# Optimization experiments

Measured on AMD Instinct MI355X. Metric: run time of the kernel, lower is better.

The kernel has to match this reference:

```python
import jax, jax.numpy as jnp
import numpy as np

EPS = 1e-8

def setup_inputs() -> dict:
    key = jax.random.key(0)
    ks = jax.random.split(key, 7)
    B, S, H, NH, V = 4, 2048, 1024, 8, 2048
    sc = 1.0 / np.sqrt(H)
    return {
        "hidden": jax.random.normal(ks[0], (B, S, H), jnp.float32),
        "prior_w": jax.random.normal(ks[1], (H, NH), jnp.float32) * sc,
        "prior_b": jnp.zeros((NH,), jnp.float32),
        "latent_w": jax.random.normal(ks[2], (H, NH * H), jnp.float32) * sc,
        "latent_b": jnp.zeros((NH * H,), jnp.float32),
        "output_w": jax.random.normal(ks[3], (H, V), jnp.float32) * sc,
        "output_b": jnp.zeros((V,), jnp.float32),
    }

def reference(hidden, prior_w, prior_b, latent_w, latent_b, output_w, output_b):
    B, S, H = hidden.shape
    NH = prior_w.shape[1]
    # prior: sigmoid then renormalize over heads
    prior = jax.nn.sigmoid(hidden @ prior_w + prior_b)              # [B,S,NH]
    prior = prior / (prior.sum(-1, keepdims=True) + EPS)
    # latent: linear -> [B,S,NH,H] -> tanh
    latent = jnp.tanh((hidden @ latent_w + latent_b).reshape(B, S, NH, H))
    # per-head softmax over vocab, weighted sum over heads
    logits = jnp.einsum('bsnh,hv->bsnv', latent, output_w) + output_b
    probs = jax.nn.softmax(logits, axis=-1)                          # [B,S,NH,V]
    return jnp.einsum('bsn,bsnv->bsv', prior, probs)
```

## Files before the change

kernel.cpp:

```cpp
#include <hip/hip_runtime.h>
#include <hip/hip_bf16.h>
#include <stdint.h>

typedef _Float16 f16;
typedef _Float16 f16x8 __attribute__((ext_vector_type(8)));
typedef _Float16 f16x4 __attribute__((ext_vector_type(4)));
typedef float f32x4 __attribute__((ext_vector_type(4)));

#define T_TOK 8192
#define H_DIM 1024
#define NHEAD 8
#define V_DIM 2048

__device__ __forceinline__ void gload16(const void* g, void* l) {
  __builtin_amdgcn_global_load_lds(
      (const __attribute__((address_space(1))) void*)(uintptr_t)g,
      (__attribute__((address_space(3))) void*)(unsigned)(uintptr_t)l,
      16, 0, 0);
}

__device__ __forceinline__ float fast_tanh(float x) {
  float xc = fminf(fmaxf(x, -12.f), 12.f);
  float e = __expf(2.f * xc);
  return (e - 1.f) / (e + 1.f);
}

__device__ __forceinline__ void stage_half(const f16* __restrict__ gRowBase,
                                           char* ldsHalf, int tid, int sl8,
                                           int Kd) {
  const int srow = tid >> 3;
  char* wuni = ldsHalf + ((tid >> 6) << 10);
  gload16(gRowBase + (size_t)srow * Kd + sl8, wuni);
  gload16(gRowBase + (size_t)(srow + 64) * Kd + sl8, wuni + 8192);
}

template <int TANH>
__global__ __launch_bounds__(512, 2) void k_gemm(const f16* __restrict__ A,
                                                 const f16* __restrict__ Bt,
                                                 const float* __restrict__ bias,
                                                 f16* __restrict__ C,
                                                 int M, int N, int K) {
  __shared__ __align__(16) f16 sA[2][16384];
  __shared__ __align__(16) f16 sB[2][16384];
  const int tid = threadIdx.x;
  const int lane = tid & 63;
  const int wid = tid >> 6;
  const int wr = wid >> 2, wc = wid & 3;
  const int m0 = blockIdx.y * 256, n0 = blockIdx.x * 256;
  const int NT = K >> 6;
  const int sl8 = ((tid & 7) ^ ((tid >> 3) & 7)) << 3;
  const int lo15 = lane & 15;
  const int offk0 = lo15 * 128 + (((lane >> 4)) ^ (lane & 7)) * 16;
  const int offk1 = lo15 * 128 + ((4 + (lane >> 4)) ^ (lane & 7)) * 16;

  const f16* Ag = A + (size_t)m0 * K;
  const f16* Bg = Bt + (size_t)n0 * K;
  char* sAb = (char*)&sA[0][0];
  char* sBb = (char*)&sB[0][0];

  stage_half(Ag, sAb, tid, sl8, K);
  stage_half(Ag + (size_t)128 * K, sAb + 16384, tid, sl8, K);
  stage_half(Bg, sBb, tid, sl8, K);
  stage_half(Bg + (size_t)128 * K, sBb + 16384, tid, sl8, K);
  stage_half(Bg + 64, sBb + 32768, tid, sl8, K);
  stage_half(Bg + (size_t)128 * K + 64, sBb + 32768 + 16384, tid, sl8, K);
  asm volatile("s_waitcnt vmcnt(4)" ::: "memory");
  __builtin_amdgcn_s_barrier();
  __builtin_amdgcn_sched_barrier(0);

  f32x4 acc[8][4] = {};
  f16x8 bf[4][2];

#define PHASE(q, STAGE_STMT)                                                   \
  {                                                                            \
    f16x8 af[2];                                                               \
    f16x8 af1[2];                                                              \
    if (q == 0) {                                                              \
      _Pragma("unroll") for (int ni = 0; ni < 4; ++ni) {                       \
        bf[ni][0] = *(const f16x8*)(cB + wc * 8192 + ni * 2048 + offk0);       \
        bf[ni][1] = *(const f16x8*)(cB + wc * 8192 + ni * 2048 + offk1);       \
      }                                                                        \
    }                                                                          \
    af[0] = *(const f16x8*)(cA + wr * 16384 + (2 * q + 0) * 2048 + offk0);     \
    af[1] = *(const f16x8*)(cA + wr * 16384 + (2 * q + 0) * 2048 + offk1);     \
    af1[0] = *(const f16x8*)(cA + wr * 16384 + (2 * q + 1) * 2048 + offk0);    \
    af1[1] = *(const f16x8*)(cA + wr * 16384 + (2 * q + 1) * 2048 + offk1);    \
    STAGE_STMT;                                                                \
    __builtin_amdgcn_s_barrier();                                              \
    asm volatile("s_waitcnt lgkmcnt(0)" ::: "memory");                         \
    __builtin_amdgcn_sched_barrier(0);                                         \
    __builtin_amdgcn_s_setprio(1);                                             \
    _Pragma("unroll") for (int ni = 0; ni < 4; ++ni) {                         \
      acc[2 * q + 0][ni] = __builtin_amdgcn_mfma_f32_16x16x32_f16(             \
          af[0], bf[ni][0], acc[2 * q + 0][ni], 0, 0, 0);                      \
      acc[2 * q + 0][ni] = __builtin_amdgcn_mfma_f32_16x16x32_f16(             \
          af[1], bf[ni][1], acc[2 * q + 0][ni], 0, 0, 0);                      \
      acc[2 * q + 1][ni] = __builtin_amdgcn_mfma_f32_16x16x32_f16(             \
          af1[0], bf[ni][0], acc[2 * q + 1][ni], 0, 0, 0);                     \
      acc[2 * q + 1][ni] = __builtin_amdgcn_mfma_f32_16x16x32_f16(             \
          af1[1], bf[ni][1], acc[2 * q + 1][ni], 0, 0, 0);                     \
    }                                                                          \
    __builtin_amdgcn_s_setprio(0);                                             \
  }

#pragma unroll 2
  for (int T = 0; T < NT; ++T) {
    const int buf = T & 1;
    const char* cA = sAb + buf * 32768;
    const char* cB = sBb + buf * 32768;
    char* nA = sAb + (buf ^ 1) * 32768;
    char* nB = sBb + buf * 32768;
    const int ktA = (T + 1) << 6;
    const int ktB = (T + 2) << 6;

    PHASE(0, { if (T + 1 < NT) stage_half(Ag + ktA, nA, tid, sl8, K); })
    __builtin_amdgcn_s_barrier();
    PHASE(1, { if (T + 1 < NT) stage_half(Ag + (size_t)128 * K + ktA, nA + 16384, tid, sl8, K); })
    __builtin_amdgcn_s_barrier();
    PHASE(2, { if (T + 2 < NT) stage_half(Bg + ktB, nB, tid, sl8, K); })
    __builtin_amdgcn_s_barrier();
    PHASE(3, { if (T + 2 < NT) stage_half(Bg + (size_t)128 * K + ktB, nB + 16384, tid, sl8, K); })
    if (T + 2 < NT) {
      asm volatile("s_waitcnt vmcnt(4)" ::: "memory");
    } else {
      asm volatile("s_waitcnt vmcnt(0)" ::: "memory");
    }
    __builtin_amdgcn_s_barrier();
    __builtin_amdgcn_sched_barrier(0);
  }
#undef PHASE

  const int crow = m0 + wr * 128 + ((lane >> 4) << 2);
  const int ccol0 = n0 + wc * 64 + lo15;
#pragma unroll
  for (int ni = 0; ni < 4; ++ni) {
    const int col = ccol0 + ni * 16;
    const float bv = bias[col];
#pragma unroll
    for (int mi = 0; mi < 8; ++mi) {
#pragma unroll
      for (int r = 0; r < 4; ++r) {
        float v = acc[mi][ni][r] + bv;
        if (TANH) v = fast_tanh(v);
        C[(size_t)(crow + mi * 16 + r) * N + col] = (f16)v;
      }
    }
  }
}

__global__ __launch_bounds__(256) void k_convert(const float* __restrict__ in,
                                                 f16* __restrict__ out, int n4) {
  int i = blockIdx.x * blockDim.x + threadIdx.x;
  if (i >= n4) return;
  const float4 v = ((const float4*)in)[i];
  f16x4 o;
  o[0] = (f16)v.x; o[1] = (f16)v.y; o[2] = (f16)v.z; o[3] = (f16)v.w;
  ((f16x4*)out)[i] = o;
}

__global__ void k_transpose(const float* __restrict__ in, f16* __restrict__ out,
                            int R, int C) {
  __shared__ f16 tile[32][33];
  int c0 = blockIdx.x * 32, r0 = blockIdx.y * 32;
  for (int j = threadIdx.y; j < 32; j += 8)
    tile[j][threadIdx.x] = (f16)in[(size_t)(r0 + j) * C + (c0 + threadIdx.x)];
  __syncthreads();
  for (int j = threadIdx.y; j < 32; j += 8)
    out[(size_t)(c0 + j) * R + (r0 + threadIdx.x)] = tile[threadIdx.x][j];
}

__global__ __launch_bounds__(256) void k_prior(const float* __restrict__ hidden,
                                               const float* __restrict__ pw,
                                               const float* __restrict__ pb,
                                               float* __restrict__ prior) {
  const int wid = threadIdx.x >> 6, lane = threadIdx.x & 63;
  const int t = blockIdx.x * 4 + wid;
  float acc[NHEAD] = {0.f, 0.f, 0.f, 0.f, 0.f, 0.f, 0.f, 0.f};
  const float* hrow = hidden + (size_t)t * H_DIM;
  for (int k = lane; k < H_DIM; k += 64) {
    float x = hrow[k];
    const float* wr = pw + k * NHEAD;
#pragma unroll
    for (int h = 0; h < NHEAD; ++h) acc[h] += x * wr[h];
  }
#pragma unroll
  for (int h = 0; h < NHEAD; ++h) {
#pragma unroll
    for (int off = 32; off >= 1; off >>= 1) acc[h] += __shfl_xor(acc[h], off);
  }
  if (lane == 0) {
    float p[NHEAD], s = 0.f;
#pragma unroll
    for (int h = 0; h < NHEAD; ++h) {
      p[h] = 1.f / (1.f + __expf(-(acc[h] + pb[h])));
      s += p[h];
    }
    float inv = 1.f / (s + 1e-8f);
#pragma unroll
    for (int h = 0; h < NHEAD; ++h) prior[t * NHEAD + h] = p[h] * inv;
  }
}

__global__ __launch_bounds__(256) void k_softmax(const f16* __restrict__ logits,
                                                 const float* __restrict__ prior,
                                                 float* __restrict__ out) {
  __shared__ float red[4];
  const int t = blockIdx.x;
  const int tid = threadIdx.x, lane = tid & 63, wid = tid >> 6;
  float oa[8] = {0.f, 0.f, 0.f, 0.f, 0.f, 0.f, 0.f, 0.f};
  const int v0 = tid * 8;
#pragma unroll 1
  for (int h = 0; h < NHEAD; ++h) {
    f16x8 x = *(const f16x8*)(logits + ((size_t)t * NHEAD + h) * V_DIM + v0);
    float xv[8], mx = -1e30f;
#pragma unroll
    for (int j = 0; j < 8; j++) { xv[j] = (float)x[j]; mx = fmaxf(mx, xv[j]); }
#pragma unroll
    for (int off = 32; off >= 1; off >>= 1) mx = fmaxf(mx, __shfl_xor(mx, off));
    if (lane == 0) red[wid] = mx;
    __syncthreads();
    mx = fmaxf(fmaxf(red[0], red[1]), fmaxf(red[2], red[3]));
    __syncthreads();
    float e[8], s = 0.f;
#pragma unroll
    for (int j = 0; j < 8; j++) { e[j] = __expf(xv[j] - mx); s += e[j]; }
#pragma unroll
    for (int off = 32; off >= 1; off >>= 1) s += __shfl_xor(s, off);
    if (lane == 0) red[wid] = s;
    __syncthreads();
    s = red[0] + red[1] + red[2] + red[3];
    __syncthreads();
    const float coef = prior[t * NHEAD + h] / s;
#pragma unroll
    for (int j = 0; j < 8; j++) oa[j] += coef * e[j];
  }
  float4* op = (float4*)(out + (size_t)t * V_DIM + v0);
  op[0] = make_float4(oa[0], oa[1], oa[2], oa[3]);
  op[1] = make_float4(oa[4], oa[5], oa[6], oa[7]);
}

extern "C" void kernel_launch(void* const* d_in, const int* in_sizes, int n_in,
                              void* d_out, int out_size, void* d_ws, size_t ws_size,
                              hipStream_t stream) {
  const float* hidden   = (const float*)d_in[0];
  const float* prior_w  = (const float*)d_in[1];
  const float* prior_b  = (const float*)d_in[2];
  const float* latent_w = (const float*)d_in[3];
  const float* latent_b = (const float*)d_in[4];
  const float* output_w = (const float*)d_in[5];
  const float* output_b = (const float*)d_in[6];
  float* out = (float*)d_out;

  char* ws = (char*)d_ws;
  size_t off = 0;
  auto alloc = [&](size_t bytes) -> void* {
    void* p = ws + off;
    off += (bytes + 255) & ~(size_t)255;
    return p;
  };
  f16* hidden_h = (f16*)alloc((size_t)T_TOK * H_DIM * 2);
  f16* lw_t     = (f16*)alloc((size_t)NHEAD * H_DIM * H_DIM * 2);
  f16* ow_t     = (f16*)alloc((size_t)V_DIM * H_DIM * 2);
  float* prior  = (float*)alloc((size_t)T_TOK * NHEAD * 4);

  int tc = 2048;
  while (tc > 256) {
    size_t need = off + (size_t)tc * NHEAD * H_DIM * 2 + 256 +
                  (size_t)tc * NHEAD * V_DIM * 2 + 256;
    if (need <= ws_size) break;
    tc >>= 1;
  }
  f16* latent_h = (f16*)alloc((size_t)tc * NHEAD * H_DIM * 2);
  f16* logits_h = (f16*)alloc((size_t)tc * NHEAD * V_DIM * 2);

  k_convert<<<(T_TOK * H_DIM / 4 + 255) / 256, 256, 0, stream>>>(
      hidden, hidden_h, T_TOK * H_DIM / 4);
  k_transpose<<<dim3(NHEAD * H_DIM / 32, H_DIM / 32), dim3(32, 8), 0, stream>>>(
      latent_w, lw_t, H_DIM, NHEAD * H_DIM);
  k_transpose<<<dim3(V_DIM / 32, H_DIM / 32), dim3(32, 8), 0, stream>>>(
      output_w, ow_t, H_DIM, V_DIM);
  k_prior<<<T_TOK / 4, 256, 0, stream>>>(hidden, prior_w, prior_b, prior);

  const int nchunk = T_TOK / tc;
  for (int c = 0; c < nchunk; ++c) {
    const f16* Ah = hidden_h + (size_t)c * tc * H_DIM;
    k_gemm<1><<<dim3(NHEAD * H_DIM / 256, tc / 256), 512, 0, stream>>>(
        Ah, lw_t, latent_b, latent_h, tc, NHEAD * H_DIM, H_DIM);
    k_gemm<0><<<dim3(V_DIM / 256, tc * NHEAD / 256), 512, 0, stream>>>(
        latent_h, ow_t, output_b, logits_h, tc * NHEAD, V_DIM, H_DIM);
    k_softmax<<<tc, 256, 0, stream>>>(logits_h, prior + (size_t)c * tc * NHEAD,
                                      out + (size_t)c * tc * V_DIM);
  }
}
```

Before: 625.5 us.

## Software-pipeline LDS fragment loads across MFMA phases and swizzle block order

Restructures the GEMM main loop so the A fragments for the next phase are read from LDS while the current phase's MFMAs run, using double register sets (af0/af1), with the next tile's first A set prefetched after the tile barrier. This removes the per-phase lgkmcnt(0) wait that previously stalled the MFMAs. It also remaps block IDs with a stride-8 swizzle, intended to improve L2 locality across XCDs, and reorders the epilogue stores row-major. The cost is higher register pressure from the extra fragment set, and the loop assumes an even number of K tiles.

```diff
diff --git a/kernel.cpp b/kernel.cpp
--- a/kernel.cpp
+++ b/kernel.cpp
@@ -46,7 +46,11 @@
   const int lane = tid & 63;
   const int wid = tid >> 6;
   const int wr = wid >> 2, wc = wid & 3;
-  const int m0 = blockIdx.y * 256, n0 = blockIdx.x * 256;
+  const int gx = gridDim.x;
+  const int id = blockIdx.y * gx + blockIdx.x;
+  const int cpx = (gx * gridDim.y) >> 3;
+  const int sw = (id & 7) * cpx + (id >> 3);
+  const int m0 = (sw / gx) * 256, n0 = (sw % gx) * 256;
   const int NT = K >> 6;
   const int sl8 = ((tid & 7) ^ ((tid >> 3) & 7)) << 3;
   const int lo15 = lane & 15;
@@ -69,80 +73,106 @@
   __builtin_amdgcn_sched_barrier(0);
 
   f32x4 acc[8][4] = {};
-  f16x8 bf[4][2];
-
-#define PHASE(q, STAGE_STMT)                                                   \
+  f16x8 af0[4], af1[4], bf[4][2];
+
+#define LDA_SET(dst, base, q)                                                  \
   {                                                                            \
-    f16x8 af[2];                                                               \
-    f16x8 af1[2];                                                              \
-    if (q == 0) {                                                              \
-      _Pragma("unroll") for (int ni = 0; ni < 4; ++ni) {                       \
-        bf[ni][0] = *(const f16x8*)(cB + wc * 8192 + ni * 2048 + offk0);       \
-        bf[ni][1] = *(const f16x8*)(cB + wc * 8192 + ni * 2048 + offk1);       \
-      }                                                                        \
+    dst[0] = *(const f16x8*)((base) + wr * 16384 + (2 * (q) + 0) * 2048 + offk0); \
+    dst[1] = *(const f16x8*)((base) + wr * 16384 + (2 * (q) + 0) * 2048 + offk1); \
+    dst[2] = *(const f16x8*)((base) + wr * 16384 + (2 * (q) + 1) * 2048 + offk0); \
+    dst[3] = *(const f16x8*)((base) + wr * 16384 + (2 * (q) + 1) * 2048 + offk1); \
+  }
+#define LDB(base)                                                              \
+  {                                                                            \
+    _Pragma("unroll") for (int ni = 0; ni < 4; ++ni) {                         \
+      bf[ni][0] = *(const f16x8*)((base) + wc * 8192 + ni * 2048 + offk0);     \
+      bf[ni][1] = *(const f16x8*)((base) + wc * 8192 + ni * 2048 + offk1);     \
     }                                                                          \
-    af[0] = *(const f16x8*)(cA + wr * 16384 + (2 * q + 0) * 2048 + offk0);     \
-    af[1] = *(const f16x8*)(cA + wr * 16384 + (2 * q + 0) * 2048 + offk1);     \
-    af1[0] = *(const f16x8*)(cA + wr * 16384 + (2 * q + 1) * 2048 + offk0);    \
-    af1[1] = *(const f16x8*)(cA + wr * 16384 + (2 * q + 1) * 2048 + offk1);    \
-    STAGE_STMT;                                                                \
-    __builtin_amdgcn_s_barrier();                                              \
-    asm volatile("s_waitcnt lgkmcnt(0)" ::: "memory");                         \
-    __builtin_amdgcn_sched_barrier(0);                                         \
+  }
+#define MFMA16(q, S)                                                           \
+  {                                                                            \
     __builtin_amdgcn_s_setprio(1);                                             \
     _Pragma("unroll") for (int ni = 0; ni < 4; ++ni) {                         \
-      acc[2 * q + 0][ni] = __builtin_amdgcn_mfma_f32_16x16x32_f16(             \
-          af[0], bf[ni][0], acc[2 * q + 0][ni], 0, 0, 0);                      \
-      acc[2 * q + 0][ni] = __builtin_amdgcn_mfma_f32_16x16x32_f16(             \
-          af[1], bf[ni][1], acc[2 * q + 0][ni], 0, 0, 0);                      \
-      acc[2 * q + 1][ni] = __builtin_amdgcn_mfma_f32_16x16x32_f16(             \
-          af1[0], bf[ni][0], acc[2 * q + 1][ni], 0, 0, 0);                     \
-      acc[2 * q + 1][ni] = __builtin_amdgcn_mfma_f32_16x16x32_f16(             \
-          af1[1], bf[ni][1], acc[2 * q + 1][ni], 0, 0, 0);                     \
+      acc[2 * (q) + 0][ni] = __builtin_amdgcn_mfma_f32_16x16x32_f16(           \
+          S[0], bf[ni][0], acc[2 * (q) + 0][ni], 0, 0, 0);                     \
+      acc[2 * (q) + 0][ni] = __builtin_amdgcn_mfma_f32_16x16x32_f16(           \
+          S[1], bf[ni][1], acc[2 * (q) + 0][ni], 0, 0, 0);                     \
+      acc[2 * (q) + 1][ni] = __builtin_amdgcn_mfma_f32_16x16x32_f16(           \
+          S[2], bf[ni][0], acc[2 * (q) + 1][ni], 0, 0, 0);                     \
+      acc[2 * (q) + 1][ni] = __builtin_amdgcn_mfma_f32_16x16x32_f16(           \
+          S[3], bf[ni][1], acc[2 * (q) + 1][ni], 0, 0, 0);                     \
     }                                                                          \
     __builtin_amdgcn_s_setprio(0);                                             \
   }
 
-#pragma unroll 2
-  for (int T = 0; T < NT; ++T) {
-    const int buf = T & 1;
-    const char* cA = sAb + buf * 32768;
-    const char* cB = sBb + buf * 32768;
-    char* nA = sAb + (buf ^ 1) * 32768;
-    char* nB = sBb + buf * 32768;
-    const int ktA = (T + 1) << 6;
-    const int ktB = (T + 2) << 6;
-
-    PHASE(0, { if (T + 1 < NT) stage_half(Ag + ktA, nA, tid, sl8, K); })
-    __builtin_amdgcn_s_barrier();
-    PHASE(1, { if (T + 1 < NT) stage_half(Ag + (size_t)128 * K + ktA, nA + 16384, tid, sl8, K); })
-    __builtin_amdgcn_s_barrier();
-    PHASE(2, { if (T + 2 < NT) stage_half(Bg + ktB, nB, tid, sl8, K); })
-    __builtin_amdgcn_s_barrier();
-    PHASE(3, { if (T + 2 < NT) stage_half(Bg + (size_t)128 * K + ktB, nB + 16384, tid, sl8, K); })
-    if (T + 2 < NT) {
-      asm volatile("s_waitcnt vmcnt(4)" ::: "memory");
-    } else {
-      asm volatile("s_waitcnt vmcnt(0)" ::: "memory");
-    }
-    __builtin_amdgcn_s_barrier();
-    __builtin_amdgcn_sched_barrier(0);
-  }
-#undef PHASE
+  LDA_SET(af0, sAb, 0);
+
+#define HALF(tt, bc)                                                           \
+  {                                                                            \
+    const char* cA = sAb + (bc)*32768;                                         \
+    const char* cB = sBb + (bc)*32768;                                         \
+    char* nA = sAb + ((bc) ^ 1) * 32768;                                       \
+    char* nB = sBb + (bc)*32768;                                               \
+    const int ktA = ((tt) + 1) << 6, ktB = ((tt) + 2) << 6;                    \
+    const bool doA = (tt) + 1 < NT, doB = (tt) + 2 < NT;                       \
+                                    \
+    if (doA) stage_half(Ag + ktA, nA, tid, sl8, K);                            \
+    LDB(cB);                                                                   \
+    LDA_SET(af1, cA, 1);                                                       \
+    __builtin_amdgcn_sched_barrier(0);                                         \
+    MFMA16(0, af0);                                                            \
+    __builtin_amdgcn_s_barrier();                                              \
+                                                                      \
+    if (doA) stage_half(Ag + (size_t)128 * K + ktA, nA + 16384, tid, sl8, K);  \
+    LDA_SET(af0, cA, 2);                                                       \
+    __builtin_amdgcn_sched_barrier(0);                                         \
+    MFMA16(1, af1);                                                            \
+    __builtin_amdgcn_s_barrier();                                              \
+                                                                      \
+    if (doB) stage_half(Bg + ktB, nB, tid, sl8, K);                            \
+    LDA_SET(af1, cA, 3);                                                       \
+    __builtin_amdgcn_sched_barrier(0);                                         \
+    MFMA16(2, af0);                                                            \
+    __builtin_amdgcn_s_barrier();                                              \
+                  \
+    if (doB) stage_half(Bg + (size_t)128 * K + ktB, nB + 16384, tid, sl8, K);  \
+    if (doB) {                                                                 \
+      asm volatile("s_waitcnt vmcnt(4)" ::: "memory");                         \
+    } else {                                                                   \
+      asm volatile("s_waitcnt vmcnt(0)" ::: "memory");                         \
+    }                                                                          \
+    __builtin_amdgcn_s_barrier();                                              \
+    __builtin_amdgcn_sched_barrier(0);                                         \
+    if (doA) LDA_SET(af0, sAb + ((bc) ^ 1) * 32768, 0);                        \
+    __builtin_amdgcn_sched_barrier(0);                                         \
+    MFMA16(3, af1);                                                            \
+  }
+
+#pragma unroll 1
+  for (int T = 0; T < NT; T += 2) {
+    HALF(T, 0);
+    HALF(T + 1, 1);
+  }
+#undef HALF
+#undef LDA_SET
+#undef LDB
+#undef MFMA16
 
   const int crow = m0 + wr * 128 + ((lane >> 4) << 2);
   const int ccol0 = n0 + wc * 64 + lo15;
-#pragma unroll
-  for (int ni = 0; ni < 4; ++ni) {
-    const int col = ccol0 + ni * 16;
-    const float bv = bias[col];
-#pragma unroll
-    for (int mi = 0; mi < 8; ++mi) {
-#pragma unroll
-      for (int r = 0; r < 4; ++r) {
-        float v = acc[mi][ni][r] + bv;
+  float bv[4];
+#pragma unroll
+  for (int ni = 0; ni < 4; ++ni) bv[ni] = bias[ccol0 + ni * 16];
+#pragma unroll
+  for (int mi = 0; mi < 8; ++mi) {
+#pragma unroll
+    for (int r = 0; r < 4; ++r) {
+      f16* Crow = C + (size_t)(crow + mi * 16 + r) * N;
+#pragma unroll
+      for (int ni = 0; ni < 4; ++ni) {
+        float v = acc[mi][ni][r] + bv[ni];
         if (TANH) v = fast_tanh(v);
-        C[(size_t)(crow + mi * 16 + r) * N + col] = (f16)v;
+        Crow[ccol0 + ni * 16] = (f16)v;
       }
     }
   }
```

Result: faster. 583.0 us (-6.8%).
